# Optimization experiments

Hardware: AMD Instinct MI355X
Metric: run time of the kernel (lower is better)

Reference implementation:

```python
import jax, jax.numpy as jnp
import numpy as np

B, N, E = 4, 160, 200000
D_EDGE, D_ORI, D_TYPE = 128, 8, 120      # d_edge, d_ori_edge, d_edge_type = d_edge - d_ori_edge
D_EXT = 512                               # d_edge * expansion_factor(4)
D_H4 = 512                                # d_edge * 4
D_REL = 16
PML, ETN = 32, 16                         # path_max_length, edge_type_num


def setup_inputs() -> dict:
    key = jax.random.key(0)
    ks = jax.random.split(key, 16)
    p = lambda i, shape, s=0.05: (jax.random.normal(ks[i], shape) * s).astype(jnp.float32)
    return dict(
        rel_type=jax.random.randint(ks[0], (E,), 0, ETN),
        rel_error=jax.random.normal(ks[1], (E, D_ORI), jnp.float32),
        edge_pos=jax.random.randint(ks[2], (E,), 0, PML),
        dist=jax.random.randint(ks[3], (B, N, N), 0, PML),
        rel_row=jnp.sort(jax.random.randint(ks[4], (E,), 0, B * N * N)),
        rel_col=jax.random.randint(ks[5], (E,), 0, 10000),
        batch_num=B, max_node=N,
        type_tab=p(6, (ETN, D_TYPE), 1.0),
        pos_tab=p(7, (PML, D_EDGE), 1.0),
        dist_tab=p(8, (PML, D_EXT), 1.0),
        w1=p(9, (D_EDGE, 2 * D_EDGE)), b1=jnp.zeros(2 * D_EDGE, jnp.float32),
        w2=p(10, (2 * D_EDGE, 4 * D_EDGE)), b2=jnp.zeros(4 * D_EDGE, jnp.float32),
        w3=p(11, (4 * D_EDGE, D_EXT)), b3=jnp.zeros(D_EXT, jnp.float32),
        g1=jnp.ones(D_EXT, jnp.float32), be1=jnp.zeros(D_EXT, jnp.float32),
        wf1=p(12, (D_EXT, D_H4)), bf1=jnp.zeros(D_H4, jnp.float32),
        g2=jnp.ones(D_H4, jnp.float32), be2=jnp.zeros(D_H4, jnp.float32),
        wf2=p(13, (D_H4, D_H4)), bf2=jnp.zeros(D_H4, jnp.float32),
        g3=jnp.ones(D_H4, jnp.float32), be3=jnp.zeros(D_H4, jnp.float32),
        wf3=p(14, (D_H4, D_REL)), bf3=jnp.zeros(D_REL, jnp.float32),
    )


def _ln(x, g, b, eps=1e-5):
    m = x.mean(-1, keepdims=True)
    v = ((x - m) ** 2).mean(-1, keepdims=True)
    return (x - m) * jax.lax.rsqrt(v + eps) * g + b


def reference(rel_type, rel_error, edge_pos, dist, rel_row, rel_col, batch_num, max_node,
              type_tab, pos_tab, dist_tab,
              w1, b1, w2, b2, w3, b3,
              g1, be1, wf1, bf1, g2, be2, wf2, bf2, g3, be3, wf3, bf3):
    type_tab = type_tab.at[0].set(0.0)   # padding_idx=0
    dist_tab = dist_tab.at[0].set(0.0)   # padding_idx=0
    # embed + concat + positional add  -> [E, D_EDGE]
    e = jnp.concatenate([type_tab[rel_type], rel_error], axis=1) + pos_tab[edge_pos]
    # point-net style edge MLP -> [E, D_EXT]
    h = jax.nn.relu(e @ w1 + b1)
    h = jax.nn.relu(h @ w2 + b2)
    h = h @ w3 + b3
    # sparse scatter-max over the hybrid-COO row index (torch_sparse.reduce.max, dim=1)
    n_seg = batch_num * max_node * max_node
    seg = jax.ops.segment_max(h, rel_row, num_segments=n_seg, indices_are_sorted=True)
    seg = jnp.where(jnp.isneginf(seg), 0.0, seg)   # empty rows -> 0 (torch_scatter fill)
    rel = seg.reshape(batch_num, max_node, max_node, -1) + dist_tab[dist]
    # fc: ReLU, LN, Linear, ReLU, LN, Linear, ReLU, LN, Linear
    x = _ln(jax.nn.relu(rel), g1, be1) @ wf1 + bf1
    x = _ln(jax.nn.relu(x), g2, be2) @ wf2 + bf2
    x = _ln(jax.nn.relu(x), g3, be3) @ wf3 + bf3   # [B, N, N, D_REL]
    # triu over the (N, N) dims, then symmetrize
    mask = jnp.triu(jnp.ones((max_node, max_node), x.dtype))
    x = x * mask[None, :, :, None]
    return x + x.transpose(0, 2, 1, 3)
```

## Files before the change

kernel.cpp:

```cpp
#include <hip/hip_runtime.h>

typedef __attribute__((ext_vector_type(8))) _Float16 half8;
typedef __attribute__((ext_vector_type(4))) _Float16 half4;
typedef __attribute__((ext_vector_type(4))) float f32x4;

constexpr int Bn = 4;
constexpr int Nn = 160;
constexpr int SEGN = Bn * Nn * Nn;
constexpr int TRIN = Nn * (Nn + 1) / 2;
constexpr int CMPN = Bn * TRIN;
constexpr int SCAN_NB = (SEGN + 511) / 512;

__device__ __forceinline__ int tri_base(int i) { return i * Nn - (i * (i - 1)) / 2; }

__global__ void k_prep(const float* __restrict__ w1, const float* __restrict__ w2,
                       const float* __restrict__ w3, const float* __restrict__ wf1,
                       const float* __restrict__ wf2, const float* __restrict__ wf3,
                       _Float16* __restrict__ o1, _Float16* __restrict__ o2,
                       _Float16* __restrict__ o3, _Float16* __restrict__ of1,
                       _Float16* __restrict__ of2, _Float16* __restrict__ of3) {
  int t = blockIdx.x * 256 + threadIdx.x;
  const float* src; _Float16* dst; int N, local; bool is3 = false;
  if (t < 32768)       { src = w1;  dst = o1;  N = 256; local = t; }
  else if (t < 163840) { src = w2;  dst = o2;  N = 512; local = t - 32768; }
  else if (t < 425984) { src = w3;  dst = o3;  N = 512; local = t - 163840; }
  else if (t < 688128) { src = wf1; dst = of1; N = 512; local = t - 425984; }
  else if (t < 950272) { src = wf2; dst = of2; N = 512; local = t - 688128; }
  else if (t < 958464) { src = wf3; dst = of3; N = 16;  local = t - 950272; is3 = true; }
  else return;
  int k = local / N;
  int n = local - k * N;
  if (is3) dst[n * 512 + k] = (_Float16)src[local];
  else dst[(size_t)((k >> 5) * N + n) * 32 + (k & 31)] = (_Float16)src[local];
}

__device__ __forceinline__ int lower_bound_rr(const int* __restrict__ rel_row, int E, int key) {
  int lo = 0, hi = E;
  while (lo < hi) { int mid = (lo + hi) >> 1; if (rel_row[mid] < key) lo = mid + 1; else hi = mid; }
  return lo;
}

__global__ void k_cnt(const int* __restrict__ rel_row, int* __restrict__ row_ptr,
                      int* __restrict__ cnt, int* __restrict__ tri2ij, int E) {
  int r = blockIdx.x * 256 + threadIdx.x;
  if (r < TRIN) {
    int lo = 0, hi = Nn - 1;
    while (lo < hi) { int mid = (lo + hi + 1) >> 1; if (tri_base(mid) <= r) lo = mid; else hi = mid - 1; }
    int j = lo + (r - tri_base(lo));
    tri2ij[r] = (lo << 16) | j;
  }
  if (r > SEGN) return;
  int lo = lower_bound_rr(rel_row, E, r);
  row_ptr[r] = lo;
  if (r < SEGN) {
    int hi2 = lower_bound_rr(rel_row, E, r + 1);
    int jj = r % Nn;
    int ii = (r / Nn) % Nn;
    cnt[r] = (ii <= jj) ? (hi2 - lo) : 0;
  }
}

__global__ void k_scan1(const int* __restrict__ cnt, int* __restrict__ pre,
                        int* __restrict__ bsum) {
  __shared__ int tmp[512];
  int t = threadIdx.x, b = blockIdx.x;
  int idx = b * 512 + t;
  int v = (idx < SEGN) ? cnt[idx] : 0;
  tmp[t] = v;
  __syncthreads();
  for (int o = 1; o < 512; o <<= 1) {
    int add = (t >= o) ? tmp[t - o] : 0;
    __syncthreads();
    tmp[t] += add;
    __syncthreads();
  }
  if (idx < SEGN) pre[idx] = tmp[t] - v;
  if (t == 511) bsum[b] = tmp[511];
}

__global__ void k_scan2(int* __restrict__ bsum, int* __restrict__ ek) {
  __shared__ int tmp[256];
  int t = threadIdx.x;
  int v = (t < SCAN_NB) ? bsum[t] : 0;
  tmp[t] = v;
  __syncthreads();
  for (int o = 1; o < 256; o <<= 1) {
    int add = (t >= o) ? tmp[t - o] : 0;
    __syncthreads();
    tmp[t] += add;
    __syncthreads();
  }
  if (t < SCAN_NB) bsum[t] = tmp[t] - v;
  if (t == 255) ek[0] = tmp[255];
}

__global__ void k_map(const int* __restrict__ row_ptr, const int* __restrict__ cnt,
                      const int* __restrict__ pre, const int* __restrict__ bsum,
                      int* __restrict__ cstart, int* __restrict__ edge_map) {
  int r = blockIdx.x * 512 + threadIdx.x;
  if (r >= SEGN) return;
  int cs = pre[r] + bsum[r >> 9];
  cstart[r] = cs;
  int c = cnt[r];
  int rp = row_ptr[r];
  for (int k = 0; k < c; ++k) edge_map[cs + k] = rp + k;
  if (r == SEGN - 1) cstart[SEGN] = cs + c;
}

template <int MT, int K, int C0, int CN, int NSTRIDE, int NT, bool SP>
__device__ __forceinline__ void do_slice(const _Float16* __restrict__ wt,
                                         const char* a_base, int nbase,
                                         f32x4 (&acc)[MT][NT], int tid) {
  constexpr int rowB = K * 2;
  const int w = tid >> 6, lane = tid & 63, ln15 = lane & 15, kg = lane >> 4;
  const char* wb = (const char*)wt;
#pragma unroll
  for (int c = 0; c < CN; ++c) {
    half8 a[MT], b[NT];
#pragma unroll
    for (int nt = 0; nt < NT; ++nt) {
      int n = nbase + (w * NT + nt) * 16 + ln15;
      b[nt] = *(const half8*)(wb + (size_t)(C0 + c) * (NSTRIDE * 64) + n * 64 + kg * 16);
    }
#pragma unroll
    for (int mt = 0; mt < MT; ++mt) {
      int row = mt * 16 + ln15;
      int byte = (row * rowB + c * 64 + kg * 16) ^ ((row & 7) << 4);
      a[mt] = *(const half8*)(a_base + byte);
    }
    if (SP) __builtin_amdgcn_s_setprio(1);
#pragma unroll
    for (int mt = 0; mt < MT; ++mt)
#pragma unroll
      for (int nt = 0; nt < NT; ++nt)
        acc[mt][nt] = __builtin_amdgcn_mfma_f32_16x16x32_f16(a[mt], b[nt], acc[mt][nt], 0, 0, 0);
    if (SP) __builtin_amdgcn_s_setprio(0);
  }
}

template <int MT, int NT>
__device__ __forceinline__ void init_accn(const float* __restrict__ bias, int nbase,
                                          f32x4 (&acc)[MT][NT], int tid) {
  const int w = tid >> 6, ln15 = tid & 15;
#pragma unroll
  for (int nt = 0; nt < NT; ++nt) {
    float bv = bias[nbase + (w * NT + nt) * 16 + ln15];
    f32x4 s = {bv, bv, bv, bv};
#pragma unroll
    for (int mt = 0; mt < MT; ++mt) acc[mt][nt] = s;
  }
}

template <int MT, int NT, bool RELU>
__device__ __forceinline__ void store_hn(char* h, int rowB, int nbase,
                                         const f32x4 (&acc)[MT][NT], int tid) {
  const int w = tid >> 6, lane = tid & 63, ln15 = lane & 15, kg = lane >> 4;
#pragma unroll
  for (int mt = 0; mt < MT; ++mt)
#pragma unroll
    for (int nt = 0; nt < NT; ++nt)
#pragma unroll
      for (int j = 0; j < 4; ++j) {
        int row = mt * 16 + kg * 4 + j;
        int n = nbase + (w * NT + nt) * 16 + ln15;
        float v = acc[mt][nt][j];
        if (RELU) v = fmaxf(v, 0.f);
        *(_Float16*)(h + ((row * rowB + n * 2) ^ ((row & 7) << 4))) = (_Float16)v;
      }
}

__global__ __launch_bounds__(512, 2) void k_edge(
    const int* __restrict__ rel_type, const float* __restrict__ rel_error,
    const int* __restrict__ edge_pos, const int* __restrict__ edge_map,
    const int* __restrict__ ekp,
    const float* __restrict__ type_tab, const float* __restrict__ pos_tab,
    const _Float16* __restrict__ w1t, const float* __restrict__ b1,
    const _Float16* __restrict__ w2t, const float* __restrict__ b2,
    const _Float16* __restrict__ w3t, const float* __restrict__ b3,
    _Float16* __restrict__ h3) {
  __shared__ __align__(16) char smem[65536];
  char* e  = smem;
  char* h1 = smem + 32768;
  char* h2 = smem;

  const int tid = threadIdx.x;
  const int e0 = blockIdx.x * 64;
  const int EK = ekp[0];
  if (e0 >= EK) return;

  {
    int r = tid >> 3, c0 = (tid & 7) * 16;
    int re = edge_map[min(e0 + r, EK - 1)];
    int rt = rel_type[re];
    int ep = edge_pos[re];
#pragma unroll
    for (int s = 0; s < 2; ++s) {
      half8 hv;
#pragma unroll
      for (int q = 0; q < 8; ++q) {
        int cc = c0 + s * 8 + q;
        float v = (cc < 120) ? (rt ? type_tab[rt * 120 + cc] : 0.f)
                             : rel_error[(size_t)re * 8 + (cc - 120)];
        v += pos_tab[ep * 128 + cc];
        hv[q] = (_Float16)v;
      }
      int byte = (r * 256 + (c0 + s * 8) * 2) ^ ((r & 7) << 4);
      *(half8*)(e + byte) = hv;
    }
  }
  __syncthreads();

  {
    f32x4 acc[4][2];
    init_accn<4, 2>(b1, 0, acc, tid);
    do_slice<4, 128, 0, 4, 256, 2, true>(w1t, e, 0, acc, tid);
    store_hn<4, 2, true>(h1, 512, 0, acc, tid);
  }
  __syncthreads();
  {
    f32x4 acc[4][4];
    init_accn<4, 4>(b2, 0, acc, tid);
    do_slice<4, 256, 0, 8, 512, 4, true>(w2t, h1, 0, acc, tid);
    __syncthreads();
    store_hn<4, 4, true>(h2, 1024, 0, acc, tid);
  }
  __syncthreads();
  {
    f32x4 acc[4][4];
    init_accn<4, 4>(b3, 0, acc, tid);
    do_slice<4, 512, 0, 16, 512, 4, true>(w3t, h2, 0, acc, tid);
    __syncthreads();
    store_hn<4, 4, false>(h2, 1024, 0, acc, tid);
    __syncthreads();
    uint4* dst = (uint4*)(h3 + (size_t)e0 * 512);
#pragma unroll
    for (int i = 0; i < 8; ++i) {
      int cidx = tid + i * 512;
      int byteoff = cidx * 16;
      int row = byteoff >> 10;
      uint4 v = *(const uint4*)(h2 + (byteoff ^ ((row & 7) << 4)));
      if (e0 + row < EK) dst[cidx] = v;
    }
  }
}

__global__ __launch_bounds__(256) void k_gather(
    const _Float16* __restrict__ h3, const int* __restrict__ cstart,
    const int* __restrict__ tri2ij, const int* __restrict__ dist,
    const float* __restrict__ dist_tab,
    const float* __restrict__ g1, const float* __restrict__ be1,
    _Float16* __restrict__ rowsA) {
  const int w = threadIdx.x >> 6, lane = threadIdx.x & 63;
  const int coff = lane * 8;
  const float* gp = g1 + coff;
  const float* bp = be1 + coff;
  const _Float16 NEGH = (_Float16)(-65504.f);
  const int pbase = blockIdx.x * 32 + w * 8;
  for (int rr = 0; rr < 8; ++rr) {
    int p = pbase + rr;
    if (p >= CMPN) return;
    int b = p / TRIN;
    int ij = tri2ij[p - b * TRIN];
    int gr = (b * Nn + (ij >> 16)) * Nn + (ij & 0xffff);
    int s = cstart[gr], en = cstart[gr + 1];
    int di = dist[gr];
    half8 mx;
#pragma unroll
    for (int q = 0; q < 8; ++q) mx[q] = NEGH;
    int idx = s;
    while (idx + 4 <= en) {
      half8 c0 = *(const half8*)(h3 + (size_t)(idx + 0) * 512 + coff);
      half8 c1 = *(const half8*)(h3 + (size_t)(idx + 1) * 512 + coff);
      half8 c2 = *(const half8*)(h3 + (size_t)(idx + 2) * 512 + coff);
      half8 c3 = *(const half8*)(h3 + (size_t)(idx + 3) * 512 + coff);
      mx = __builtin_elementwise_max(mx, __builtin_elementwise_max(
               __builtin_elementwise_max(c0, c1), __builtin_elementwise_max(c2, c3)));
      idx += 4;
    }
    if (idx + 2 <= en) {
      half8 c0 = *(const half8*)(h3 + (size_t)(idx + 0) * 512 + coff);
      half8 c1 = *(const half8*)(h3 + (size_t)(idx + 1) * 512 + coff);
      mx = __builtin_elementwise_max(mx, __builtin_elementwise_max(c0, c1));
      idx += 2;
    }
    if (idx < en) {
      half8 c0 = *(const half8*)(h3 + (size_t)idx * 512 + coff);
      mx = __builtin_elementwise_max(mx, c0);
    }
    const float* dt = dist_tab + (size_t)di * 512 + coff;
    float v[8]; float s1 = 0.f, s2 = 0.f;
#pragma unroll
    for (int q = 0; q < 8; ++q) {
      float vv = (s == en) ? 0.f : (float)mx[q];
      if (di) vv += dt[q];
      vv = fmaxf(vv, 0.f);
      v[q] = vv; s1 += vv; s2 += vv * vv;
    }
#pragma unroll
    for (int o = 32; o > 0; o >>= 1) { s1 += __shfl_xor(s1, o); s2 += __shfl_xor(s2, o); }
    float mean = s1 * (1.f / 512.f);
    float rs = rsqrtf(s2 * (1.f / 512.f) - mean * mean + 1e-5f);
    half8 ov;
#pragma unroll
    for (int q = 0; q < 8; ++q) ov[q] = (_Float16)((v[q] - mean) * rs * gp[q] + bp[q]);
    *(half8*)((char*)rowsA + (size_t)p * 1024 + ((coff * 2) ^ ((p & 7) << 4))) = ov;
  }
}

__device__ __forceinline__ void epi_ln_store(f32x4 (&acc)[4][4], char* dst,
                                             float* st1, float* st2,
                                             float* stM, float* stR,
                                             const float* __restrict__ g,
                                             const float* __restrict__ be, int tid) {
  const int w = tid >> 6, lane = tid & 63, ln15 = lane & 15, kg = lane >> 4;
#pragma unroll
  for (int mt = 0; mt < 4; ++mt)
#pragma unroll
    for (int nt = 0; nt < 4; ++nt)
#pragma unroll
      for (int j = 0; j < 4; ++j) acc[mt][nt][j] = fmaxf(acc[mt][nt][j], 0.f);
#pragma unroll
  for (int mt = 0; mt < 4; ++mt)
#pragma unroll
    for (int j = 0; j < 4; ++j) {
      float a = 0.f, b = 0.f;
#pragma unroll
      for (int nt = 0; nt < 4; ++nt) { float v = acc[mt][nt][j]; a += v; b += v * v; }
#pragma unroll
      for (int m = 1; m < 16; m <<= 1) { a += __shfl_xor(a, m); b += __shfl_xor(b, m); }
      if (ln15 == 0) {
        int r = mt * 16 + kg * 4 + j;
        st1[w * 64 + r] = a;
        st2[w * 64 + r] = b;
      }
    }
  __syncthreads();
  if (tid < 64) {
    float a = 0.f, b = 0.f;
#pragma unroll
    for (int ww = 0; ww < 8; ++ww) { a += st1[ww * 64 + tid]; b += st2[ww * 64 + tid]; }
    float mean = a * (1.f / 512.f);
    float var = b * (1.f / 512.f) - mean * mean;
    stM[tid] = mean;
    stR[tid] = rsqrtf(var + 1e-5f);
  }
  __syncthreads();
  float gv[4], bv[4];
#pragma unroll
  for (int nt = 0; nt < 4; ++nt) {
    int n = (w * 4 + nt) * 16 + ln15;
    gv[nt] = g[n]; bv[nt] = be[n];
  }
#pragma unroll
  for (int mt = 0; mt < 4; ++mt)
#pragma unroll
    for (int j = 0; j < 4; ++j) {
      int r = mt * 16 + kg * 4 + j;
      float mean = stM[r], rs = stR[r];
#pragma unroll
      for (int nt = 0; nt < 4; ++nt) {
        int n = (w * 4 + nt) * 16 + ln15;
        float v = (acc[mt][nt][j] - mean) * rs * gv[nt] + bv[nt];
        *(_Float16*)(dst + ((r * 1024 + n * 2) ^ ((r & 7) << 4))) = (_Float16)v;
      }
    }
  __syncthreads();
}

__global__ __launch_bounds__(512, 2) void k_fcg(
    const _Float16* __restrict__ rowsA,
    const float* __restrict__ g2, const float* __restrict__ be2,
    const _Float16* __restrict__ wf1t, const float* __restrict__ bf1,
    const float* __restrict__ g3, const float* __restrict__ be3,
    const _Float16* __restrict__ wf2t, const float* __restrict__ bf2,
    const _Float16* __restrict__ wf3t, const float* __restrict__ bf3,
    float* __restrict__ x3c) {
  __shared__ __align__(16) char bufA[65536];
  __shared__ float st1[512], st2[512];
  __shared__ float stM[64], stR[64];

  const int tid = threadIdx.x;
  const int p0 = blockIdx.x * 64;

  {
    const uint4* src = (const uint4*)((const char*)rowsA + (size_t)p0 * 1024);
    uint4* dst = (uint4*)bufA;
#pragma unroll
    for (int i = 0; i < 8; ++i) dst[tid + i * 512] = src[tid + i * 512];
  }
  __syncthreads();

  {
    f32x4 acc[4][4];
    init_accn<4, 4>(bf1, 0, acc, tid);
    do_slice<4, 512, 0, 16, 512, 4, true>(wf1t, bufA, 0, acc, tid);
    epi_ln_store(acc, bufA, st1, st2, stM, stR, g2, be2, tid);
  }
  {
    f32x4 acc[4][4];
    init_accn<4, 4>(bf2, 0, acc, tid);
    do_slice<4, 512, 0, 16, 512, 4, true>(wf2t, bufA, 0, acc, tid);
    epi_ln_store(acc, bufA, st1, st2, stM, stR, g3, be3, tid);
  }
  {
    const int w = tid >> 6, lane = tid & 63, ln15 = lane & 15, kg = lane >> 4;
    if (w < 4) {
      f32x4 acc3 = {0.f, 0.f, 0.f, 0.f};
#pragma unroll
      for (int c = 0; c < 16; ++c) {
        half8 b = *(const half8*)((const char*)wf3t + ln15 * 1024 + c * 64 + kg * 16);
        int row = w * 16 + ln15;
        half8 a = *(const half8*)(bufA + ((row * 1024 + c * 64 + kg * 16) ^ ((row & 7) << 4)));
        acc3 = __builtin_amdgcn_mfma_f32_16x16x32_f16(a, b, acc3, 0, 0, 0);
      }
#pragma unroll
      for (int j = 0; j < 4; ++j)
        x3c[(size_t)(p0 + w * 16 + kg * 4 + j) * 16 + ln15] = acc3[j] + bf3[ln15];
    }
  }
}

__global__ void k_sym(const float* __restrict__ x3c, float* __restrict__ out) {
  int t = blockIdx.x * 256 + threadIdx.x;
  if (t >= SEGN * 4) return;
  int q = t & 3;
  int cell = t >> 2;
  int j = cell % Nn;
  int tmp = cell / Nn;
  int i = tmp % Nn;
  int b = tmp / Nn;
  int lo = min(i, j), hi = i ^ j ^ lo;
  int p = b * TRIN + tri_base(lo) + (hi - lo);
  float4 v = *(const float4*)&x3c[(size_t)p * 16 + q * 4];
  if (i == j) { v.x *= 2.f; v.y *= 2.f; v.z *= 2.f; v.w *= 2.f; }
  *(float4*)&out[(size_t)t * 4] = v;
}

extern "C" void kernel_launch(void* const* d_in, const int* in_sizes, int n_in,
                              void* d_out, int out_size, void* d_ws, size_t ws_size,
                              hipStream_t stream) {
  const int*   rel_type  = (const int*)d_in[0];
  const float* rel_error = (const float*)d_in[1];
  const int*   edge_pos  = (const int*)d_in[2];
  const int*   dist      = (const int*)d_in[3];
  const int*   rel_row   = (const int*)d_in[4];
  const float* type_tab = (const float*)d_in[8];
  const float* pos_tab  = (const float*)d_in[9];
  const float* dist_tab = (const float*)d_in[10];
  const float* w1 = (const float*)d_in[11]; const float* b1 = (const float*)d_in[12];
  const float* w2 = (const float*)d_in[13]; const float* b2 = (const float*)d_in[14];
  const float* w3 = (const float*)d_in[15]; const float* b3 = (const float*)d_in[16];
  const float* g1 = (const float*)d_in[17]; const float* be1 = (const float*)d_in[18];
  const float* wf1 = (const float*)d_in[19]; const float* bf1 = (const float*)d_in[20];
  const float* g2 = (const float*)d_in[21]; const float* be2 = (const float*)d_in[22];
  const float* wf2 = (const float*)d_in[23]; const float* bf2 = (const float*)d_in[24];
  const float* g3 = (const float*)d_in[25]; const float* be3 = (const float*)d_in[26];
  const float* wf3 = (const float*)d_in[27]; const float* bf3 = (const float*)d_in[28];

  const int E = in_sizes[0];
  const size_t h3_bytes   = (size_t)E * 512 * 2;
  const size_t rows_off   = ((size_t)E * 55 / 100) * 1024;
  const size_t x3_bytes   = (size_t)CMPN * 16 * 4;
  const size_t ptr_bytes  = (size_t)(SEGN + 1) * 4;
  const size_t tri_bytes  = (size_t)TRIN * 4;
  const size_t cell_bytes = (size_t)SEGN * 4;
  const size_t cst_bytes  = (size_t)(SEGN + 1) * 4;
  const size_t map_bytes  = (size_t)E * 4;
  const size_t wt_elems   = 32768 + 131072 + 262144 * 3 + 8192;
  const size_t total = h3_bytes + x3_bytes + ptr_bytes + tri_bytes + 2 * cell_bytes +
                       cst_bytes + map_bytes + 1024 + 256 * 4 + wt_elems * 2;
  if (ws_size < total) return;

  char* wp = (char*)d_ws;
  _Float16* h3      = (_Float16*)wp;
  _Float16* rowsA   = (_Float16*)(wp + rows_off);
  wp += h3_bytes;
  float*    x3c     = (float*)wp;               wp += x3_bytes;
  int*      row_ptr = (int*)wp;                 wp += ptr_bytes;
  int*      tri2ij  = (int*)wp;                 wp += tri_bytes;
  int*      cnt     = (int*)wp;                 wp += cell_bytes;
  int*      pre     = (int*)wp;                 wp += cell_bytes;
  int*      cstart  = (int*)wp;                 wp += cst_bytes;
  int*      edge_map= (int*)wp;                 wp += map_bytes;
  int*      bsum    = (int*)wp;                 wp += 256 * 4;
  int*      ekp     = (int*)wp;                 wp += 1024;
  _Float16* w1t     = (_Float16*)wp;
  _Float16* w2t  = w1t + 32768;
  _Float16* w3t  = w2t + 131072;
  _Float16* wf1t = w3t + 262144;
  _Float16* wf2t = wf1t + 262144;
  _Float16* wf3t = wf2t + 262144;
  float*    out  = (float*)d_out;

  k_prep<<<3744, 256, 0, stream>>>(w1, w2, w3, wf1, wf2, wf3,
                                   w1t, w2t, w3t, wf1t, wf2t, wf3t);
  k_cnt<<<(SEGN + 256) / 256, 256, 0, stream>>>(rel_row, row_ptr, cnt, tri2ij, E);
  k_scan1<<<SCAN_NB, 512, 0, stream>>>(cnt, pre, bsum);
  k_scan2<<<1, 256, 0, stream>>>(bsum, ekp);
  k_map<<<SCAN_NB, 512, 0, stream>>>(row_ptr, cnt, pre, bsum, cstart, edge_map);
  k_edge<<<(E + 63) / 64, 512, 0, stream>>>(rel_type, rel_error, edge_pos, edge_map, ekp,
                                            type_tab, pos_tab, w1t, b1, w2t, b2, w3t, b3,
                                            h3);
  k_gather<<<(CMPN + 31) / 32, 256, 0, stream>>>(h3, cstart, tri2ij, dist, dist_tab,
                                                 g1, be1, rowsA);
  k_fcg<<<CMPN / 64, 512, 0, stream>>>(rowsA,
                                       g2, be2, wf1t, bf1,
                                       g3, be3, wf2t, bf2,
                                       wf3t, bf3, x3c);
  k_sym<<<(SEGN * 4 + 255) / 256, 256, 0, stream>>>(x3c, out);
}
```

Measured before the change: 375.6 us.

## Double k_edge tile to 128 edges per 1024-thread block for weight reuse

The edge MLP kernel now handles 128 edges per block with 16 waves instead of 64 edges with 8 waves, using 128 KB of LDS. A new slice routine has each wave cover all 128 rows against a narrower set of output columns. Each weight fragment loaded from global memory is therefore reused across twice as many rows, roughly halving weight traffic per edge. The cost is one large block per CU rather than two, which gives coarser scheduling, larger barrier groups and a bigger tail effect on the last wave of blocks.

```diff
diff --git a/kernel.cpp b/kernel.cpp
--- a/kernel.cpp
+++ b/kernel.cpp
@@ -138,6 +138,44 @@
   }
 }
 
+template <int K, int NTW>
+__device__ __forceinline__ void do_slice8(const _Float16* __restrict__ wt,
+                                          const char* a_base,
+                                          f32x4 (&acc)[8][NTW], int tid) {
+  constexpr int C = K / 32;
+  constexpr int N = NTW * 256;
+  constexpr int rowB = K * 2;
+  const int w = tid >> 6, lane = tid & 63, ln15 = lane & 15, kg = lane >> 4;
+  const char* wb = (const char*)wt;
+#pragma unroll
+  for (int c = 0; c < C; ++c) {
+    half8 b[NTW];
+#pragma unroll
+    for (int nt = 0; nt < NTW; ++nt) {
+      int n = (w * NTW + nt) * 16 + ln15;
+      b[nt] = *(const half8*)(wb + (size_t)c * (N * 64) + n * 64 + kg * 16);
+    }
+#pragma unroll
+    for (int mh = 0; mh < 2; ++mh) {
+      half8 a[4];
+#pragma unroll
+      for (int mt = 0; mt < 4; ++mt) {
+        int row = mh * 64 + mt * 16 + ln15;
+        int byte = (row * rowB + c * 64 + kg * 16) ^ ((row & 7) << 4);
+        a[mt] = *(const half8*)(a_base + byte);
+      }
+      __builtin_amdgcn_s_setprio(1);
+#pragma unroll
+      for (int mt = 0; mt < 4; ++mt)
+#pragma unroll
+        for (int nt = 0; nt < NTW; ++nt)
+          acc[mh * 4 + mt][nt] =
+              __builtin_amdgcn_mfma_f32_16x16x32_f16(a[mt], b[nt], acc[mh * 4 + mt][nt], 0, 0, 0);
+      __builtin_amdgcn_s_setprio(0);
+    }
+  }
+}
+
 template <int MT, int NT>
 __device__ __forceinline__ void init_accn(const float* __restrict__ bias, int nbase,
                                           f32x4 (&acc)[MT][NT], int tid) {
@@ -169,7 +207,7 @@
       }
 }
 
-__global__ __launch_bounds__(512, 2) void k_edge(
+__global__ __launch_bounds__(1024, 1) void k_edge(
     const int* __restrict__ rel_type, const float* __restrict__ rel_error,
     const int* __restrict__ edge_pos, const int* __restrict__ edge_map,
     const int* __restrict__ ekp,
@@ -178,13 +216,13 @@
     const _Float16* __restrict__ w2t, const float* __restrict__ b2,
     const _Float16* __restrict__ w3t, const float* __restrict__ b3,
     _Float16* __restrict__ h3) {
-  __shared__ __align__(16) char smem[65536];
+  __shared__ __align__(16) char smem[131072];
   char* e  = smem;
-  char* h1 = smem + 32768;
+  char* h1 = smem + 65536;
   char* h2 = smem;
 
   const int tid = threadIdx.x;
-  const int e0 = blockIdx.x * 64;
+  const int e0 = blockIdx.x * 128;
   const int EK = ekp[0];
   if (e0 >= EK) return;
 
@@ -211,31 +249,31 @@
   __syncthreads();
 
   {
-    f32x4 acc[4][2];
-    init_accn<4, 2>(b1, 0, acc, tid);
-    do_slice<4, 128, 0, 4, 256, 2, true>(w1t, e, 0, acc, tid);
-    store_hn<4, 2, true>(h1, 512, 0, acc, tid);
-  }
-  __syncthreads();
-  {
-    f32x4 acc[4][4];
-    init_accn<4, 4>(b2, 0, acc, tid);
-    do_slice<4, 256, 0, 8, 512, 4, true>(w2t, h1, 0, acc, tid);
-    __syncthreads();
-    store_hn<4, 4, true>(h2, 1024, 0, acc, tid);
-  }
-  __syncthreads();
-  {
-    f32x4 acc[4][4];
-    init_accn<4, 4>(b3, 0, acc, tid);
-    do_slice<4, 512, 0, 16, 512, 4, true>(w3t, h2, 0, acc, tid);
-    __syncthreads();
-    store_hn<4, 4, false>(h2, 1024, 0, acc, tid);
+    f32x4 acc[8][1];
+    init_accn<8, 1>(b1, 0, acc, tid);
+    do_slice8<128, 1>(w1t, e, acc, tid);
+    store_hn<8, 1, true>(h1, 512, 0, acc, tid);
+  }
+  __syncthreads();
+  {
+    f32x4 acc[8][2];
+    init_accn<8, 2>(b2, 0, acc, tid);
+    do_slice8<256, 2>(w2t, h1, acc, tid);
+    __syncthreads();
+    store_hn<8, 2, true>(h2, 1024, 0, acc, tid);
+  }
+  __syncthreads();
+  {
+    f32x4 acc[8][2];
+    init_accn<8, 2>(b3, 0, acc, tid);
+    do_slice8<512, 2>(w3t, h2, acc, tid);
+    __syncthreads();
+    store_hn<8, 2, false>(h2, 1024, 0, acc, tid);
     __syncthreads();
     uint4* dst = (uint4*)(h3 + (size_t)e0 * 512);
 #pragma unroll
     for (int i = 0; i < 8; ++i) {
-      int cidx = tid + i * 512;
+      int cidx = tid + i * 1024;
       int byteoff = cidx * 16;
       int row = byteoff >> 10;
       uint4 v = *(const uint4*)(h2 + (byteoff ^ ((row & 7) << 4)));
@@ -498,9 +536,9 @@
   k_scan1<<<SCAN_NB, 512, 0, stream>>>(cnt, pre, bsum);
   k_scan2<<<1, 256, 0, stream>>>(bsum, ekp);
   k_map<<<SCAN_NB, 512, 0, stream>>>(row_ptr, cnt, pre, bsum, cstart, edge_map);
-  k_edge<<<(E + 63) / 64, 512, 0, stream>>>(rel_type, rel_error, edge_pos, edge_map, ekp,
-                                            type_tab, pos_tab, w1t, b1, w2t, b2, w3t, b3,
-                                            h3);
+  k_edge<<<(E + 127) / 128, 1024, 0, stream>>>(rel_type, rel_error, edge_pos, edge_map, ekp,
+                                               type_tab, pos_tab, w1t, b1, w2t, b2, w3t, b3,
+                                               h3);
   k_gather<<<(CMPN + 31) / 32, 256, 0, stream>>>(h3, cstart, tri2ij, dist, dist_tab,
                                                  g1, be1, rowsA);
   k_fcg<<<CMPN / 64, 512, 0, stream>>>(rowsA,
```

Result: slower. 477.3 us (+27.1%).
